# Performance work log

Measured on AMD Instinct MI355X. Metric: run time of the kernel, lower is better.

The kernel has to match this reference:

```python
import jax, jax.numpy as jnp
import numpy as np

B, T, CIN = 32, 16384, 32
COUT, NB, NA = 32, 3, 2


def setup_inputs() -> dict:
    key = jax.random.key(0)
    k1, k2, k3, k4 = jax.random.split(key, 4)
    u = jax.random.normal(k1, (B, T, CIN), dtype=jnp.float32)
    x0 = jax.random.normal(k2, (B, NA, COUT), dtype=jnp.float32)
    # AR coeffs scaled small so the length-16384 IIR recurrence is stable
    a_coeff = jax.random.normal(k3, (NA, COUT), dtype=jnp.float32) * 0.05
    b_coeff = jax.random.normal(k4, (NB, CIN, COUT), dtype=jnp.float32)
    return {"u": u, "x0": x0, "a_coeff": a_coeff, "b_coeff": b_coeff}


def reference(u, x0, a_coeff, b_coeff):
    # u: [B, T, CIN], x0: [B, NA, COUT]
    b, t, cin = u.shape
    n_a, cout = a_coeff.shape
    n_b = b_coeff.shape[0]
    a_f = jnp.flip(a_coeff, axis=0)   # [NA, COUT]
    b_f = jnp.flip(b_coeff, axis=0)   # [NB, CIN, COUT]

    def step(carry, ut):
        ubuf, xbuf = carry                                   # [NB,B,CIN], [NA,B,COUT]
        ubuf = jnp.concatenate([ubuf[1:], ut[None]], axis=0)  # push current input
        xt = jnp.einsum('to,tbo->bo', a_f, xbuf) + jnp.einsum('tio,tbi->bo', b_f, ubuf)
        xbuf = jnp.concatenate([xbuf[1:], xt[None]], axis=0)
        return (ubuf, xbuf), xt

    u0 = jnp.zeros((n_b, b, cin), dtype=u.dtype)
    x0_t = jnp.transpose(x0, (1, 0, 2))                      # [NA, B, COUT]
    _, ys = jax.lax.scan(step, (u0, x0_t), jnp.transpose(u, (1, 0, 2)), unroll=3)
    return jnp.transpose(ys, (1, 0, 2))                      # [B, T, COUT]
```

## Files before the change

kernel.cpp:

```cpp
#include <hip/hip_runtime.h>
#include <hip/hip_bf16.h>

namespace {

typedef short bf16x8 __attribute__((ext_vector_type(8), may_alias));
typedef float f32x4_ma __attribute__((ext_vector_type(4), may_alias));
typedef __attribute__((ext_vector_type(16))) float f32x16;

constexpr int kB = 32, kT = 16384, kCin = 32, kCout = 32;
constexpr int kL = 128;
constexpr int kK = 32;
constexpr int kChunks = kT / kL;
constexpr int kWpB = 4;
constexpr int kRows = 34;
constexpr int kStageF = kRows * kCin;
constexpr int kNT = 5;
constexpr int kTS = 36;
constexpr int kTBufF = 32 * kTS;

__device__ __forceinline__ short f2bf(float f) {
  return (short)__builtin_bit_cast(unsigned short, __float2bfloat16(f));
}

__device__ __forceinline__ void dma16(const float* g, float* l) {
  __builtin_amdgcn_global_load_lds(
      (__attribute__((address_space(1))) void*)(uintptr_t)g,
      (__attribute__((address_space(3))) void*)l, 16, 0, 0);
}

#define VMWAIT(N)                                            \
  do {                                                       \
    asm volatile("s_waitcnt vmcnt(" #N ")" ::: "memory");    \
    __builtin_amdgcn_sched_barrier(0);                       \
  } while (0)

__global__ __launch_bounds__(256, 2) void mimo_dma(
    const float* __restrict__ u,
    const float* __restrict__ x0,
    const float* __restrict__ a_coeff,
    const float* __restrict__ b_coeff,
    float* __restrict__ out)
{
  __shared__ float stg[kWpB][3][kStageF];
  __shared__ float tbf[kWpB][kTBufF];

  const int tidx = (int)threadIdx.x;
  const int lane = tidx & 63;
  const int col  = lane & 31;
  const int g    = lane >> 5;
  const int widx = tidx >> 6;
  const int wid  = (int)blockIdx.x * kWpB + widx;
  const int b     = wid >> 7;
  const int chunk = wid & (kChunks - 1);
  const int t0     = chunk * kL;
  const int tstart = t0 - kK;

  float* Tw = &tbf[widx][0];

  bf16x8 Bf[3][2];
#pragma unroll
  for (int tau = 0; tau < 3; ++tau)
#pragma unroll
    for (int h = 0; h < 2; ++h) {
      const float* bp = b_coeff + (size_t)(2 - tau) * kCin * kCout
                        + (16 * g + 8 * h) * kCout + col;
      bf16x8 fr;
#pragma unroll
      for (int j = 0; j < 8; ++j) fr[j] = f2bf(bp[j * kCout]);
      Bf[tau][h] = fr;
    }

  const float a1 = a_coeff[col];
  const float a2 = a_coeff[kCout + col];
  float i1 = 0.f, i2 = 0.f;
  if (chunk == 0) {
    i1 = x0[(b * 2 + 1) * kCout + col];
    i2 = x0[(b * 2 + 0) * kCout + col];
  }
  float s1 = 0.f, s2 = 0.f;

  const float* ub = u + (size_t)b * kT * kCin;
  float* ob = out + (size_t)b * kT * kCout;

  auto dma_stage = [&](float* buf, int rowbase) {
#pragma unroll
    for (int k = 0; k < 4; ++k) {
      const int p = k * 64 + lane;
      const int row = p >> 3;
      const int grow = rowbase + row;
      const int src = (grow < 0 ? 0 : grow) * kCin + (((p & 7) ^ (row & 7)) << 2);
      dma16(ub + src, buf + k * 256);
    }
    if (lane < 16) {
      const int p = 256 + lane;
      const int row = p >> 3;
      const int grow = rowbase + row;
      const int src = (grow < 0 ? 0 : grow) * kCin + (((p & 7) ^ (row & 7)) << 2);
      dma16(ub + src, buf + 1024);
    }
  };
  auto zero_fix = [&](float* buf, int rowbase) {
    const int nch = (-rowbase) * 8;
    for (int p = lane; p < nch; p += 64) {
      f32x4_ma z; z[0] = 0.f; z[1] = 0.f; z[2] = 0.f; z[3] = 0.f;
      *(f32x4_ma*)(buf + p * 4) = z;
    }
  };

  dma_stage(&stg[widx][0][0], tstart - 2);
  dma_stage(&stg[widx][1][0], tstart - 2 + 32);

#pragma unroll
  for (int tile = 0; tile < kNT; ++tile) {
    if (tile + 2 < kNT)
      dma_stage(&stg[widx][(tile + 2) % 3][0], tstart - 2 + 32 * (tile + 2));

    if (tile == 0)      VMWAIT(10);
    else if (tile == 1) VMWAIT(10);
    else if (tile == 2) VMWAIT(14);
    else if (tile == 3) VMWAIT(13);
    else                VMWAIT(8);

    const int rowbase = tstart - 2 + 32 * tile;
    float* Sf = &stg[widx][tile % 3][0];
    if (chunk == 0 && rowbase < 0) zero_fix(Sf, rowbase);

    f32x16 acc;
#pragma unroll
    for (int i = 0; i < 16; ++i) acc[i] = 0.f;
#pragma unroll
    for (int tau = 0; tau < 3; ++tau) {
      const int r = col + tau;
      const float* rp = Sf + r * kCin;
      const int rx = r & 7;
#pragma unroll
      for (int h = 0; h < 2; ++h) {
        const int c0 = 4 * g + 2 * h;
        const f32x4_ma lo = *(const f32x4_ma*)(rp + ((c0 ^ rx) << 2));
        const f32x4_ma hi = *(const f32x4_ma*)(rp + (((c0 + 1) ^ rx) << 2));
        bf16x8 fa;
        fa[0] = f2bf(lo[0]); fa[1] = f2bf(lo[1]);
        fa[2] = f2bf(lo[2]); fa[3] = f2bf(lo[3]);
        fa[4] = f2bf(hi[0]); fa[5] = f2bf(hi[1]);
        fa[6] = f2bf(hi[2]); fa[7] = f2bf(hi[3]);
        acc = __builtin_amdgcn_mfma_f32_32x32x16_bf16(fa, Bf[tau][h], acc, 0, 0, 0);
      }
    }

    if (chunk == 0 && tile == 1) { s1 = i1; s2 = i2; }

    const bool owned = (tile >= 1);
    const int tbase = tstart + 32 * tile;

    float x1 = s1, x2 = s2;
#pragma unroll
    for (int q = 0; q < 4; ++q) {
      const float o0 = __shfl_xor(acc[4 * q + 0], 32);
      const float o1 = __shfl_xor(acc[4 * q + 1], 32);
      const float o2 = __shfl_xor(acc[4 * q + 2], 32);
      const float o3 = __shfl_xor(acc[4 * q + 3], 32);
      const float va0 = g ? o0 : acc[4 * q + 0];
      const float va1 = g ? o1 : acc[4 * q + 1];
      const float va2 = g ? o2 : acc[4 * q + 2];
      const float va3 = g ? o3 : acc[4 * q + 3];
      const float ya0 = fmaf(a1, x1,  fmaf(a2, x2,  va0));
      const float ya1 = fmaf(a1, ya0, fmaf(a2, x1,  va1));
      const float ya2 = fmaf(a1, ya1, fmaf(a2, ya0, va2));
      const float ya3 = fmaf(a1, ya2, fmaf(a2, ya1, va3));
      const float vb0 = g ? acc[4 * q + 0] : o0;
      const float vb1 = g ? acc[4 * q + 1] : o1;
      const float vb2 = g ? acc[4 * q + 2] : o2;
      const float vb3 = g ? acc[4 * q + 3] : o3;
      const float yb0 = fmaf(a1, ya3, fmaf(a2, ya2, vb0));
      const float yb1 = fmaf(a1, yb0, fmaf(a2, ya3, vb1));
      const float yb2 = fmaf(a1, yb1, fmaf(a2, yb0, vb2));
      const float yb3 = fmaf(a1, yb2, fmaf(a2, yb1, vb3));
      x2 = yb2; x1 = yb3;
      if (owned) {
        const int rb = 8 * q + 4 * g;
        Tw[(rb + 0) * kTS + col] = g ? yb0 : ya0;
        Tw[(rb + 1) * kTS + col] = g ? yb1 : ya1;
        Tw[(rb + 2) * kTS + col] = g ? yb2 : ya2;
        Tw[(rb + 3) * kTS + col] = g ? yb3 : ya3;
      }
    }
    s1 = x1; s2 = x2;

    if (owned) {
      asm volatile("" ::: "memory");
#pragma unroll
      for (int p = 0; p < 4; ++p) {
        const f32x4_ma v = *(const f32x4_ma*)
            ((const char*)Tw + (8 * p + (lane >> 3)) * (kTS * 4) + (lane & 7) * 16);
        *(f32x4_ma*)(ob + (size_t)(tbase + 8 * p) * kCout + lane * 4) = v;
      }
      asm volatile("" ::: "memory");
    }
  }
}

}

extern "C" void kernel_launch(void* const* d_in, const int* in_sizes, int n_in,
                              void* d_out, int out_size, void* d_ws, size_t ws_size,
                              hipStream_t stream) {
  const float* u  = (const float*)d_in[0];
  const float* x0 = (const float*)d_in[1];
  const float* a  = (const float*)d_in[2];
  const float* bb = (const float*)d_in[3];
  float* out = (float*)d_out;

  dim3 grid(kB * kChunks / kWpB);
  dim3 block(256);
  hipLaunchKernelGGL(mimo_dma, grid, block, 0, stream, u, x0, a, bb, out);
}
```

Baseline: 30.07 us.

## Stage whole chunk input to LDS in one DMA burst with 2-wave blocks

```diff
diff --git a/kernel.cpp b/kernel.cpp
--- a/kernel.cpp
+++ b/kernel.cpp
@@ -11,9 +11,10 @@
 constexpr int kL = 128;
 constexpr int kK = 32;
 constexpr int kChunks = kT / kL;
-constexpr int kWpB = 4;
-constexpr int kRows = 34;
+constexpr int kWpB = 2;
+constexpr int kRows = kK + kL + 2;
 constexpr int kStageF = kRows * kCin;
+constexpr int kPos = kRows * 8;
 constexpr int kNT = 5;
 constexpr int kTS = 36;
 constexpr int kTBufF = 32 * kTS;
@@ -28,20 +29,14 @@
       (__attribute__((address_space(3))) void*)l, 16, 0, 0);
 }
 
-#define VMWAIT(N)                                            \
-  do {                                                       \
-    asm volatile("s_waitcnt vmcnt(" #N ")" ::: "memory");    \
-    __builtin_amdgcn_sched_barrier(0);                       \
-  } while (0)
-
-__global__ __launch_bounds__(256, 2) void mimo_dma(
+__global__ __launch_bounds__(128) void mimo_stream(
     const float* __restrict__ u,
     const float* __restrict__ x0,
     const float* __restrict__ a_coeff,
     const float* __restrict__ b_coeff,
     float* __restrict__ out)
 {
-  __shared__ float stg[kWpB][3][kStageF];
+  __shared__ float stg[kWpB][kStageF];
   __shared__ float tbf[kWpB][kTBufF];
 
   const int tidx = (int)threadIdx.x;
@@ -55,7 +50,30 @@
   const int t0     = chunk * kL;
   const int tstart = t0 - kK;
 
+  float* Sf = &stg[widx][0];
   float* Tw = &tbf[widx][0];
+
+  const float* ub = u + (size_t)b * kT * kCin;
+  float* ob = out + (size_t)b * kT * kCout;
+
+  {
+    const int rowbase = tstart - 2;
+#pragma unroll
+    for (int k = 0; k < kPos / 64; ++k) {
+      const int p = k * 64 + lane;
+      const int row = p >> 3;
+      const int grow = rowbase + row;
+      const int src = (grow < 0 ? 0 : grow) * kCin + (((p & 7) ^ (row & 7)) << 2);
+      dma16(ub + src, Sf + k * 256);
+    }
+    if (lane < (kPos & 63)) {
+      const int p = (kPos & ~63) + lane;
+      const int row = p >> 3;
+      const int grow = rowbase + row;
+      const int src = (grow < 0 ? 0 : grow) * kCin + (((p & 7) ^ (row & 7)) << 2);
+      dma16(ub + src, Sf + (kPos & ~63) * 4);
+    }
+  }
 
   bf16x8 Bf[3][2];
 #pragma unroll
@@ -79,60 +97,34 @@
   }
   float s1 = 0.f, s2 = 0.f;
 
-  const float* ub = u + (size_t)b * kT * kCin;
-  float* ob = out + (size_t)b * kT * kCout;
-
-  auto dma_stage = [&](float* buf, int rowbase) {
-#pragma unroll
-    for (int k = 0; k < 4; ++k) {
-      const int p = k * 64 + lane;
-      const int row = p >> 3;
-      const int grow = rowbase + row;
-      const int src = (grow < 0 ? 0 : grow) * kCin + (((p & 7) ^ (row & 7)) << 2);
-      dma16(ub + src, buf + k * 256);
-    }
-    if (lane < 16) {
-      const int p = 256 + lane;
-      const int row = p >> 3;
-      const int grow = rowbase + row;
-      const int src = (grow < 0 ? 0 : grow) * kCin + (((p & 7) ^ (row & 7)) << 2);
-      dma16(ub + src, buf + 1024);
-    }
-  };
-  auto zero_fix = [&](float* buf, int rowbase) {
-    const int nch = (-rowbase) * 8;
-    for (int p = lane; p < nch; p += 64) {
-      f32x4_ma z; z[0] = 0.f; z[1] = 0.f; z[2] = 0.f; z[3] = 0.f;
-      *(f32x4_ma*)(buf + p * 4) = z;
-    }
-  };
-
-  dma_stage(&stg[widx][0][0], tstart - 2);
-  dma_stage(&stg[widx][1][0], tstart - 2 + 32);
+  asm volatile("s_waitcnt vmcnt(0)" ::: "memory");
+  __builtin_amdgcn_sched_barrier(0);
+
+  if (chunk == 0) {
+#pragma unroll
+    for (int p0 = 0; p0 < 272; p0 += 64) {
+      const int p = p0 + lane;
+      if (p < 272) {
+        f32x4_ma z; z[0] = 0.f; z[1] = 0.f; z[2] = 0.f; z[3] = 0.f;
+        *(f32x4_ma*)(Sf + p * 4) = z;
+      }
+    }
+    asm volatile("" ::: "memory");
+  }
 
 #pragma unroll
   for (int tile = 0; tile < kNT; ++tile) {
-    if (tile + 2 < kNT)
-      dma_stage(&stg[widx][(tile + 2) % 3][0], tstart - 2 + 32 * (tile + 2));
-
-    if (tile == 0)      VMWAIT(10);
-    else if (tile == 1) VMWAIT(10);
-    else if (tile == 2) VMWAIT(14);
-    else if (tile == 3) VMWAIT(13);
-    else                VMWAIT(8);
-
-    const int rowbase = tstart - 2 + 32 * tile;
-    float* Sf = &stg[widx][tile % 3][0];
-    if (chunk == 0 && rowbase < 0) zero_fix(Sf, rowbase);
+    const int tbase = tstart + 32 * tile;
+    const bool owned = (tile >= 1);
 
     f32x16 acc;
 #pragma unroll
     for (int i = 0; i < 16; ++i) acc[i] = 0.f;
 #pragma unroll
     for (int tau = 0; tau < 3; ++tau) {
-      const int r = col + tau;
-      const float* rp = Sf + r * kCin;
-      const int rx = r & 7;
+      const int s = 32 * tile + col + tau;
+      const float* rp = Sf + s * kCin;
+      const int rx = (col + tau) & 7;
 #pragma unroll
       for (int h = 0; h < 2; ++h) {
         const int c0 = 4 * g + 2 * h;
@@ -148,9 +140,6 @@
     }
 
     if (chunk == 0 && tile == 1) { s1 = i1; s2 = i2; }
-
-    const bool owned = (tile >= 1);
-    const int tbase = tstart + 32 * tile;
 
     float x1 = s1, x2 = s2;
 #pragma unroll
@@ -211,6 +200,6 @@
   float* out = (float*)d_out;
 
   dim3 grid(kB * kChunks / kWpB);
-  dim3 block(256);
-  hipLaunchKernelGGL(mimo_dma, grid, block, 0, stream, u, x0, a, bb, out);
-}
+  dim3 block(128);
+  hipLaunchKernelGGL(mimo_stream, grid, block, 0, stream, u, x0, a, bb, out);
+}
```

After: 34.08 us. 13.3% more time.
